# Performance work log

Hardware: AMD Instinct MI355X
Metric: run time of the kernel (lower is better)

The kernel has to match this reference:

```python
import jax, jax.numpy as jnp
import numpy as np


def log_g(x):
    # log of g(x) = x+0.5 for x>=0, sigmoid(x) for x<0, computed stably
    return jnp.where(x >= 0, jnp.log(jax.nn.relu(x) + 0.5), -jax.nn.softplus(-x))


def setup_inputs() -> dict:
    key = jax.random.key(0)
    k1, k2 = jax.random.split(key)
    B, S, D = 4, 4096, 1024
    x = jax.random.normal(k1, (B, S, D), dtype=jnp.float32)
    W = jax.random.normal(k2, (D, 3 * D), dtype=jnp.float32) * (1.0 / np.sqrt(D))
    return {"x": x, "W": W}


def reference(x, W):
    # fused gate projection: [B,S,D] @ [D,3D] -> f_gate, i_gate, hidden
    gates = jnp.einsum('bsd,de->bse', x, W)
    f_gate, i_gate, hidden = jnp.split(gates, 3, axis=-1)

    # log-space normalized gates: log_f = log(sig(f)/(sig(f)+sig(i))) etc.
    diff = jax.nn.softplus(-f_gate) - jax.nn.softplus(-i_gate)
    log_f = -jax.nn.softplus(diff)
    log_i = -jax.nn.softplus(-diff)
    log_tilde_h = log_g(hidden)

    log_values = log_i + log_tilde_h
    # parallel scan in log space over seq axis (axis=1)
    a_star = jnp.cumsum(log_f, axis=1)
    log_h0_plus_b_star = jax.lax.cumlogsumexp(log_values - a_star, axis=1)
    h = jnp.exp(a_star + log_h0_plus_b_star)  # [B,S,D]
    return h  # to_out is Identity for expansion_factor == 1.0
```

## Files before the change

### kernel.cpp

```cpp
#include <hip/hip_runtime.h>
#include <hip/hip_fp16.h>
#include <cstdint>

typedef _Float16 half8  __attribute__((ext_vector_type(8)));
typedef _Float16 half4v __attribute__((ext_vector_type(4)));
typedef _Float16 half2v __attribute__((ext_vector_type(2)));
typedef float    floatx4 __attribute__((ext_vector_type(4)));

constexpr int Bb = 4, Ss = 4096, Dd = 1024;
constexpr int Mdim = Bb * Ss;
constexpr int Ndim = 3 * Dd;
constexpr int Kdim = Dd;
constexpr int CH = 256, LCH = Ss / CH;


__device__ __forceinline__ void gload_lds16(const void* g, void* l) {
  __builtin_amdgcn_global_load_lds(
      (const __attribute__((address_space(1))) uint32_t*)g,
      (__attribute__((address_space(3))) uint32_t*)l, 16, 0, 0);
}

__device__ __forceinline__ void gate_fv(float fg, float ig, float hg,
                                        float& fw, float& v) {
  float ef = __expf(fminf(-fg, 40.f));
  float ei = __expf(fminf(-ig, 40.f));
  float r  = __builtin_amdgcn_rcpf(2.f + ef + ei);
  fw = (1.f + ei) * r;
  float iw = (1.f + ef) * r;
  float g  = hg >= 0.f ? hg + 0.5f
                       : __builtin_amdgcn_rcpf(1.f + __expf(fminf(-hg, 40.f)));
  v = iw * g;
}

__global__ __launch_bounds__(256) void cvt_k(const float* __restrict__ X,
                                             _Float16* __restrict__ X16,
                                             const float* __restrict__ W,
                                             _Float16* __restrict__ WT) {
  __shared__ float tile[32][33];
  int bid = blockIdx.x;
  if (bid < 2048) {
    const int n4 = Mdim * Kdim / 4;
    for (int i = bid * 256 + threadIdx.x; i < n4; i += 2048 * 256) {
      float4 v = ((const float4*)X)[i];
      half4v o = {(_Float16)v.x, (_Float16)v.y, (_Float16)v.z, (_Float16)v.w};
      ((half4v*)X16)[i] = o;
    }
  } else {
    int b2 = bid - 2048;
    int tx = threadIdx.x & 31, ty = threadIdx.x >> 5;
    int n0 = (b2 % 96) * 32, k0 = (b2 / 96) * 32;
#pragma unroll
    for (int j = 0; j < 4; ++j) {
      int k = ty + j * 8;
      tile[k][tx] = W[(int64_t)(k0 + k) * Ndim + n0 + tx];
    }
    __syncthreads();
#pragma unroll
    for (int j = 0; j < 4; ++j) {
      int nl = ty + j * 8;
      int n = n0 + nl;
      int g = n >> 10, d = n & 1023;
      int p = (d >> 6) * 192 + g * 64 + (d & 63);
      WT[(int64_t)p * Kdim + k0 + tx] = (_Float16)tile[tx][nl];
    }
  }
}

constexpr int GBM = 128, GBN = 192, GBK = 64;
constexpr int NT = Kdim / GBK;
constexpr int LBUF = 40960;

__global__ __launch_bounds__(512, 4) void gemm8_k(const _Float16* __restrict__ A,
                                                  const _Float16* __restrict__ BT,
                                                  _Float16* __restrict__ fv,
                                                  float* __restrict__ Fc,
                                                  float* __restrict__ Hc) {
  extern __shared__ char lds[];
  const int tid = threadIdx.x;
  const int wid = tid >> 6, lane = tid & 63;
  const int wm = wid >> 2, wn = wid & 3;
  const int l15 = lane & 15, lq = lane >> 4;

  int wg = blockIdx.x;
  wg = (wg & 7) * 256 + (wg >> 3);
  const int win = wg >> 6;
  const int wi = wg & 63;
  const int m0 = (((win >> 1) << 3) + (wi >> 3)) * GBM;
  const int dp = ((win & 1) << 3) + (wi & 7);
  const int d0 = dp * 64;

  int aO[4];
#pragma unroll
  for (int mi = 0; mi < 4; ++mi) {
    int r = wm * 64 + mi * 16 + l15;
    aO[mi] = r * 128 + ((lq ^ (r & 7)) << 4);
  }
  const int rB = wn * 16 + l15;
  const int bO = rB * 128 + ((lq ^ (rB & 7)) << 4);

  const int srr = (wid << 3) + (lane >> 3);
  const int ss = lane & 7;
  const _Float16* Abase = A + (size_t)m0 * Kdim;
  const _Float16* Bbase = BT + (size_t)dp * 192 * Kdim;

  auto stage = [&](const _Float16* gsrc, int ldsBase, int nr) {
#pragma unroll
    for (int round = 0; round < 3; ++round) {
      if (round >= nr) break;
      int r = (round << 6) + srr;
      int c = ss ^ (r & 7);
      gload_lds16(gsrc + (size_t)r * Kdim + (c << 3),
                  lds + ldsBase + (round << 13) + (wid << 10));
    }
  };

  floatx4 acc[4][3] = {};

  stage(Abase, 0, 2);
  stage(Bbase, 16384, 3);
  stage(Abase + 64, LBUF, 2);
  stage(Bbase + 64, LBUF + 16384, 3);
  asm volatile("s_waitcnt vmcnt(5)" ::: "memory");
  __builtin_amdgcn_s_barrier();

  for (int kt = 0; kt < NT; ++kt) {
    const int cur = (kt & 1) * LBUF;

    half8 a[4][2], b[3][2];
#pragma unroll
    for (int mi = 0; mi < 4; ++mi)
#pragma unroll
      for (int ks = 0; ks < 2; ++ks)
        a[mi][ks] = *(const half8*)(lds + cur + (aO[mi] ^ (ks << 6)));
#pragma unroll
    for (int g = 0; g < 3; ++g)
#pragma unroll
      for (int ks = 0; ks < 2; ++ks)
        b[g][ks] = *(const half8*)(lds + cur + 16384 + (g << 13) + (bO ^ (ks << 6)));

    __builtin_amdgcn_s_setprio(1);
#pragma unroll
    for (int ks = 0; ks < 2; ++ks)
#pragma unroll
      for (int mi = 0; mi < 2; ++mi)
#pragma unroll
        for (int g = 0; g < 3; ++g)
          acc[mi][g] = __builtin_amdgcn_mfma_f32_16x16x32_f16(
              a[mi][ks], b[g][ks], acc[mi][g], 0, 0, 0);
    __builtin_amdgcn_s_setprio(0);

    __builtin_amdgcn_s_barrier();
    if (kt + 2 < NT) {
      const _Float16* Ak = Abase + (kt + 2) * GBK;
      const _Float16* Bk = Bbase + (kt + 2) * GBK;
      stage(Ak, cur, 2);
      stage(Bk, cur + 16384, 3);
    }

    __builtin_amdgcn_s_setprio(1);
#pragma unroll
    for (int ks = 0; ks < 2; ++ks)
#pragma unroll
      for (int mi = 2; mi < 4; ++mi)
#pragma unroll
        for (int g = 0; g < 3; ++g)
          acc[mi][g] = __builtin_amdgcn_mfma_f32_16x16x32_f16(
              a[mi][ks], b[g][ks], acc[mi][g], 0, 0, 0);
    __builtin_amdgcn_s_setprio(0);

    if (kt < NT - 2) {
      asm volatile("s_waitcnt vmcnt(5)" ::: "memory");
      __builtin_amdgcn_s_barrier();
    } else if (kt == NT - 2) {
      asm volatile("s_waitcnt vmcnt(0)" ::: "memory");
      __builtin_amdgcn_s_barrier();
    }
  }

  const int dcol = d0 + wn * 16 + l15;
#pragma unroll
  for (int mf = 0; mf < 4; ++mf) {
    int row0 = m0 + wm * 64 + mf * 16;
    float Fl = 1.f, Hl = 0.f;
    half8 o;
#pragma unroll
    for (int r = 0; r < 4; ++r) {
      float fw, v;
      gate_fv(acc[mf][0][r], acc[mf][1][r], acc[mf][2][r], fw, v);
      o[2 * r] = (_Float16)fw;
      o[2 * r + 1] = (_Float16)v;
      float fr = (float)o[2 * r], vr = (float)o[2 * r + 1];
      Hl = fmaf(fr, Hl, vr);
      Fl *= fr;
    }
    *(half8*)(fv + ((size_t)((row0 >> 2) + lq) * Dd + dcol) * 8) = o;
    float Fg = 1.f, Hg = 0.f;
#pragma unroll
    for (int j = 0; j < 4; ++j) {
      float Fj = __shfl(Fl, j * 16 + l15);
      float Hj = __shfl(Hl, j * 16 + l15);
      Hg = fmaf(Fj, Hg, Hj);
      Fg *= Fj;
    }
    if (lq == 0) {
      int bb = row0 >> 12, s0 = row0 & (Ss - 1);
      int co = (bb * CH + (s0 >> 4)) * Dd + dcol;
      Fc[co] = Fg;
      Hc[co] = Hg;
    }
  }
}

__global__ __launch_bounds__(256) void scan2_k(const float* __restrict__ Fc,
                                               const float* __restrict__ Hc,
                                               float* __restrict__ Carry) {
  int idx = blockIdx.x * 256 + threadIdx.x;
  int b = idx >> 10, d = idx & (Dd - 1);
  float carry = 0.f;
#pragma unroll 8
  for (int c = 0; c < CH; ++c) {
    int co = (b * CH + c) * Dd + d;
    Carry[co] = carry;
    carry = fmaf(Fc[co], carry, Hc[co]);
  }
}

__global__ __launch_bounds__(256) void scan3_k(const _Float16* __restrict__ fv,
                                               const float* __restrict__ Carry,
                                               float* __restrict__ Out) {
  int d = blockIdx.x * 256 + threadIdx.x;
  int c = blockIdx.y, b = blockIdx.z;
  int row0 = b * Ss + c * LCH;
  const _Float16* p = fv + ((size_t)(row0 >> 2) * Dd + d) * 8;
  float* o = Out + (size_t)row0 * Dd + d;
  float h = Carry[(b * CH + c) * Dd + d];
#pragma unroll
  for (int j = 0; j < 4; ++j) {
    half8 q = *(const half8*)(p + (size_t)j * Dd * 8);
#pragma unroll
    for (int r = 0; r < 4; ++r) {
      h = fmaf((float)q[2 * r], h, (float)q[2 * r + 1]);
      o[(size_t)(j * 4 + r) * Dd] = h;
    }
  }
}

extern "C" void kernel_launch(void* const* d_in, const int* in_sizes, int n_in,
                              void* d_out, int out_size, void* d_ws, size_t ws_size,
                              hipStream_t stream) {
  const float* x = (const float*)d_in[0];
  const float* W = (const float*)d_in[1];
  float* out = (float*)d_out;

  char* ws = (char*)d_ws;
  size_t off = 0;
  auto alloc = [&](size_t bytes) {
    char* p = ws + off;
    off += (bytes + 255) & ~size_t(255);
    return p;
  };
  _Float16* fv     = (_Float16*)alloc((size_t)Mdim * Dd * 2 * 2);
  float* Fc        = (float*)alloc((size_t)Bb * CH * Dd * 4);
  float* Hc        = (float*)alloc((size_t)Bb * CH * Dd * 4);
  float* Carry     = (float*)alloc((size_t)Bb * CH * Dd * 4);
  _Float16* x16    = (_Float16*)alloc((size_t)Mdim * Kdim * 2);
  _Float16* w16t   = (_Float16*)alloc((size_t)Ndim * Kdim * 2);
  if (off > ws_size) return;

  cvt_k<<<5120, 256, 0, stream>>>(x, x16, W, w16t);
  gemm8_k<<<dim3((Mdim / GBM) * (Dd / 64)), 512, 81920, stream>>>(x16, w16t, fv, Fc, Hc);
  scan2_k<<<(Bb * Dd) / 256, 256, 0, stream>>>(Fc, Hc, Carry);
  scan3_k<<<dim3(4, CH, Bb), 256, 0, stream>>>(fv, Carry, out);
}
```

Before: 173.4 us.

## Pre-pack B in MFMA fragment order and load it directly into registers

The weight conversion kernel now writes W into a layout where each wave's MFMA B fragments sit contiguously per k-tile. The GEMM loads B straight from global memory into double-buffered registers instead of staging it through LDS, which cuts LDS per block from 80 KB to 32 KB and removes the B LDS reads. This frees LDS for more resident blocks and lowers LDS traffic. In exchange, register pressure rises, and each block's B loads now go through global memory and cache without LDS sharing across the M-waves.

```diff
diff --git a/kernel.cpp b/kernel.cpp
--- a/kernel.cpp
+++ b/kernel.cpp
@@ -4,7 +4,6 @@
 
 typedef _Float16 half8  __attribute__((ext_vector_type(8)));
 typedef _Float16 half4v __attribute__((ext_vector_type(4)));
-typedef _Float16 half2v __attribute__((ext_vector_type(2)));
 typedef float    floatx4 __attribute__((ext_vector_type(4)));
 
 constexpr int Bb = 4, Ss = 4096, Dd = 1024;
@@ -35,7 +34,7 @@
 __global__ __launch_bounds__(256) void cvt_k(const float* __restrict__ X,
                                              _Float16* __restrict__ X16,
                                              const float* __restrict__ W,
-                                             _Float16* __restrict__ WT) {
+                                             _Float16* __restrict__ Bp) {
   __shared__ float tile[32][33];
   int bid = blockIdx.x;
   if (bid < 2048) {
@@ -59,19 +58,23 @@
     for (int j = 0; j < 4; ++j) {
       int nl = ty + j * 8;
       int n = n0 + nl;
+      int k = k0 + tx;
       int g = n >> 10, d = n & 1023;
-      int p = (d >> 6) * 192 + g * 64 + (d & 63);
-      WT[(int64_t)p * Kdim + k0 + tx] = (_Float16)tile[tx][nl];
+      int dp = d >> 6, wnc = (d >> 4) & 3, l15c = d & 15;
+      int kt = k >> 6, ks = (k >> 5) & 1, lqc = (k >> 3) & 3, e = k & 7;
+      size_t dst = (((size_t)(dp * 16 + kt) * 4 + wnc) * 6 + g * 2 + ks) * 512
+                 + (lqc * 16 + l15c) * 8 + e;
+      Bp[dst] = (_Float16)tile[tx][nl];
     }
   }
 }
 
 constexpr int GBM = 128, GBN = 192, GBK = 64;
 constexpr int NT = Kdim / GBK;
-constexpr int LBUF = 40960;
+constexpr int LBUF = 16384;
 
 __global__ __launch_bounds__(512, 4) void gemm8_k(const _Float16* __restrict__ A,
-                                                  const _Float16* __restrict__ BT,
+                                                  const _Float16* __restrict__ Bp,
                                                   _Float16* __restrict__ fv,
                                                   float* __restrict__ Fc,
                                                   float* __restrict__ Hc) {
@@ -95,18 +98,14 @@
     int r = wm * 64 + mi * 16 + l15;
     aO[mi] = r * 128 + ((lq ^ (r & 7)) << 4);
   }
-  const int rB = wn * 16 + l15;
-  const int bO = rB * 128 + ((lq ^ (rB & 7)) << 4);
 
   const int srr = (wid << 3) + (lane >> 3);
   const int ss = lane & 7;
   const _Float16* Abase = A + (size_t)m0 * Kdim;
-  const _Float16* Bbase = BT + (size_t)dp * 192 * Kdim;
-
-  auto stage = [&](const _Float16* gsrc, int ldsBase, int nr) {
-#pragma unroll
-    for (int round = 0; round < 3; ++round) {
-      if (round >= nr) break;
+
+  auto stageA = [&](const _Float16* gsrc, int ldsBase) {
+#pragma unroll
+    for (int round = 0; round < 2; ++round) {
       int r = (round << 6) + srr;
       int c = ss ^ (r & 7);
       gload_lds16(gsrc + (size_t)r * Kdim + (c << 3),
@@ -114,29 +113,35 @@
     }
   };
 
+  const _Float16* BpW = Bp + ((size_t)dp * 64 + wn) * 3072 + (size_t)lane * 8;
+  auto loadB = [&](int kt, half8 (&bn)[3][2]) {
+    const _Float16* p = BpW + (size_t)kt * 12288;
+#pragma unroll
+    for (int g = 0; g < 3; ++g)
+#pragma unroll
+      for (int ks = 0; ks < 2; ++ks)
+        bn[g][ks] = *(const half8*)(p + (g * 2 + ks) * 512);
+  };
+
   floatx4 acc[4][3] = {};
-
-  stage(Abase, 0, 2);
-  stage(Bbase, 16384, 3);
-  stage(Abase + 64, LBUF, 2);
-  stage(Bbase + 64, LBUF + 16384, 3);
-  asm volatile("s_waitcnt vmcnt(5)" ::: "memory");
+  half8 bA_[3][2], bB_[3][2];
+
+  stageA(Abase, 0);
+  stageA(Abase + GBK, LBUF);
+  loadB(0, bA_);
+  asm volatile("s_waitcnt vmcnt(8)" ::: "memory");
   __builtin_amdgcn_s_barrier();
 
-  for (int kt = 0; kt < NT; ++kt) {
+  auto tileStep = [&](int kt, half8 (&bc)[3][2], half8 (&bn)[3][2]) {
     const int cur = (kt & 1) * LBUF;
-
-    half8 a[4][2], b[3][2];
+    if (kt + 1 < NT) loadB(kt + 1, bn);
+
+    half8 a[4][2];
 #pragma unroll
     for (int mi = 0; mi < 4; ++mi)
 #pragma unroll
       for (int ks = 0; ks < 2; ++ks)
         a[mi][ks] = *(const half8*)(lds + cur + (aO[mi] ^ (ks << 6)));
-#pragma unroll
-    for (int g = 0; g < 3; ++g)
-#pragma unroll
-      for (int ks = 0; ks < 2; ++ks)
-        b[g][ks] = *(const half8*)(lds + cur + 16384 + (g << 13) + (bO ^ (ks << 6)));
 
     __builtin_amdgcn_s_setprio(1);
 #pragma unroll
@@ -146,16 +151,12 @@
 #pragma unroll
         for (int g = 0; g < 3; ++g)
           acc[mi][g] = __builtin_amdgcn_mfma_f32_16x16x32_f16(
-              a[mi][ks], b[g][ks], acc[mi][g], 0, 0, 0);
+              a[mi][ks], bc[g][ks], acc[mi][g], 0, 0, 0);
     __builtin_amdgcn_s_setprio(0);
 
+    asm volatile("s_waitcnt lgkmcnt(0)" ::: "memory");
     __builtin_amdgcn_s_barrier();
-    if (kt + 2 < NT) {
-      const _Float16* Ak = Abase + (kt + 2) * GBK;
-      const _Float16* Bk = Bbase + (kt + 2) * GBK;
-      stage(Ak, cur, 2);
-      stage(Bk, cur + 16384, 3);
-    }
+    if (kt + 2 < NT) stageA(Abase + (kt + 2) * GBK, cur);
 
     __builtin_amdgcn_s_setprio(1);
 #pragma unroll
@@ -165,16 +166,21 @@
 #pragma unroll
         for (int g = 0; g < 3; ++g)
           acc[mi][g] = __builtin_amdgcn_mfma_f32_16x16x32_f16(
-              a[mi][ks], b[g][ks], acc[mi][g], 0, 0, 0);
+              a[mi][ks], bc[g][ks], acc[mi][g], 0, 0, 0);
     __builtin_amdgcn_s_setprio(0);
 
     if (kt < NT - 2) {
-      asm volatile("s_waitcnt vmcnt(5)" ::: "memory");
+      asm volatile("s_waitcnt vmcnt(8)" ::: "memory");
       __builtin_amdgcn_s_barrier();
     } else if (kt == NT - 2) {
       asm volatile("s_waitcnt vmcnt(0)" ::: "memory");
       __builtin_amdgcn_s_barrier();
     }
+  };
+
+  for (int kt = 0; kt < NT; kt += 2) {
+    tileStep(kt, bA_, bB_);
+    tileStep(kt + 1, bB_, bA_);
   }
 
   const int dcol = d0 + wn * 16 + l15;
@@ -264,11 +270,11 @@
   float* Hc        = (float*)alloc((size_t)Bb * CH * Dd * 4);
   float* Carry     = (float*)alloc((size_t)Bb * CH * Dd * 4);
   _Float16* x16    = (_Float16*)alloc((size_t)Mdim * Kdim * 2);
-  _Float16* w16t   = (_Float16*)alloc((size_t)Ndim * Kdim * 2);
+  _Float16* Bp     = (_Float16*)alloc((size_t)Ndim * Kdim * 2);
   if (off > ws_size) return;
 
-  cvt_k<<<5120, 256, 0, stream>>>(x, x16, W, w16t);
-  gemm8_k<<<dim3((Mdim / GBM) * (Dd / 64)), 512, 81920, stream>>>(x16, w16t, fv, Fc, Hc);
+  cvt_k<<<5120, 256, 0, stream>>>(x, x16, W, Bp);
+  gemm8_k<<<dim3((Mdim / GBM) * (Dd / 64)), 512, 32768, stream>>>(x16, Bp, fv, Fc, Hc);
   scan2_k<<<(Bb * Dd) / 256, 256, 0, stream>>>(Fc, Hc, Carry);
   scan3_k<<<dim3(4, CH, Bb), 256, 0, stream>>>(fv, Carry, out);
 }
```

Result: slower. 295.0 us (+70.1%).
